# Performance work log

Measured on AMD Instinct MI355X. Metric: run time of the kernel, lower is better.

Reference implementation:

```python
import jax, jax.numpy as jnp
import numpy as np

PADDING = 1
STRIDE = 1


def setup_inputs() -> dict:
    key = jax.random.key(0)
    k1, k2, k3 = jax.random.split(key, 3)
    inputs = jax.random.normal(k1, (32, 128, 56, 56), dtype=jnp.float32)
    weight = jax.random.normal(k2, (256, 128, 3, 3), dtype=jnp.float32) * 0.05
    bias = jax.random.normal(k3, (256,), dtype=jnp.float32) * 0.05
    return {"inputs": inputs, "weight": weight, "bias": bias}


def reference(inputs, weight, bias):
    # Same math as unfold + matmul + fold: a standard 2D convolution
    # (cross-correlation) with bias, NCHW / OIHW layouts.
    out = jax.lax.conv_general_dilated(
        inputs, weight,
        window_strides=(STRIDE, STRIDE),
        padding=[(PADDING, PADDING), (PADDING, PADDING)],
        dimension_numbers=("NCHW", "OIHW", "NCHW"),
    )
    return out + bias[None, :, None, None]
```

## Files before the change

### kernel.cpp

```cpp
#include <hip/hip_runtime.h>
#include <hip/hip_bf16.h>


typedef __bf16 bf16x8 __attribute__((ext_vector_type(8)));
typedef float f32x4 __attribute__((ext_vector_type(4)));

#define N_IMG 32
#define C_IN 128
#define HW 56
#define K_OUT 256
#define YPAD 58
#define XPAD 64
#define IN_PAD_OFF 1048576ul

__device__ __forceinline__ void gl_lds16(const __bf16* g, __bf16* l) {
    __builtin_amdgcn_global_load_lds(
        (const __attribute__((address_space(1))) unsigned int*)(const void*)g,
        (__attribute__((address_space(3))) unsigned int*)(void*)l,
        16, 0, 0);
}

__global__ void prep_weight(const float* __restrict__ wt, __bf16* __restrict__ w2) {
    int idx = blockIdx.x * 256 + threadIdx.x;
    if (idx >= 9 * K_OUT * 16) return;
    int c8 = idx & 15;
    int ko = (idx >> 4) & 255;
    int rs = idx >> 12;
    const float* src = wt + ((size_t)ko * C_IN + c8 * 8) * 9 + rs;
    bf16x8 v8;
#pragma unroll
    for (int k = 0; k < 8; ++k) v8[k] = (__bf16)src[k * 9];
    *(bf16x8*)(w2 + (size_t)idx * 8) = v8;
}

__global__ void prep_input(const float* __restrict__ in, __bf16* __restrict__ in_pad) {
    int bid = blockIdx.x;
    int y = bid % YPAD;
    int n = bid / YPAD;
    int h = y - 1;
    bool interior = (h >= 0 && h < HW);
    __shared__ float tile[HW * 130];
    int t = threadIdx.x;
    if (interior) {
        const float* src = in + (size_t)n * C_IN * (HW * HW) + (size_t)h * HW;
#pragma unroll 1
        for (int idx = t; idx < C_IN * 14; idx += 256) {
            int c = idx / 14, g = idx % 14;
            f32x4 v = *(const f32x4*)(src + (size_t)c * (HW * HW) + g * 4);
            int w = g * 4;
            tile[(w + 0) * 130 + c] = v.x;
            tile[(w + 1) * 130 + c] = v.y;
            tile[(w + 2) * 130 + c] = v.z;
            tile[(w + 3) * 130 + c] = v.w;
        }
    }
    __syncthreads();
    __bf16* dst = in_pad + (size_t)(n * YPAD + y) * XPAD * C_IN;
#pragma unroll 1
    for (int idx = t; idx < XPAD * 16; idx += 256) {
        int x = idx >> 4, cg = idx & 15;
        bf16x8 v8;
        if (interior && x >= 1 && x <= HW) {
            const float* tp = tile + (x - 1) * 130 + cg * 8;
#pragma unroll
            for (int k = 0; k < 8; ++k) v8[k] = (__bf16)tp[k];
        } else {
#pragma unroll
            for (int k = 0; k < 8; ++k) v8[k] = (__bf16)0.f;
        }
        *(bf16x8*)(dst + x * C_IN + cg * 8) = v8;
    }
}

__global__ __launch_bounds__(256, 4) void conv_mfma(
        const __bf16* __restrict__ in_pad,
        const __bf16* __restrict__ w2,
        const float* __restrict__ bias,
        float* __restrict__ out)
{
    __shared__ __bf16 sA[8 * 16 * 64];
    __shared__ __bf16 sB[128 * 64];

    int bid  = blockIdx.x;
    int kot  = bid & 1;
    int wt_  = (bid >> 1) & 3;
    int rest = bid >> 3;
    int ht   = rest % 7;
    int n    = rest / 7;

    int h0  = ht * 8;
    int w0  = (wt_ == 3) ? 40 : wt_ * 16;
    int ko0 = kot * 128;

    int tid  = threadIdx.x;
    int lane = tid & 63;
    int wave = tid >> 6;
    int mw   = wave & 1;
    int nw   = wave >> 1;
    int l15  = lane & 15;
    int quad = lane >> 4;

    int aoff[4], boff[4];
#pragma unroll
    for (int q = 0; q < 4; ++q) {
        int chunk = q * 256 + tid;
        int i  = chunk >> 7;
        int x  = (chunk >> 3) & 15;
        int cs = chunk & 7;
        aoff[q] = (i * XPAD + x) * C_IN + (cs ^ (x & 7)) * 8;
        int ko = chunk >> 3;
        boff[q] = ko * C_IN + (cs ^ (ko & 7)) * 8;
    }

    int ac0   = quad ^ (l15 & 7);
    int aBase = (mw * 64 + l15) * 64;
    int bBase = (nw * 64 + l15) * 64;

    const __bf16* aG = in_pad + (((size_t)n * YPAD + h0) * XPAD + w0) * C_IN;
    const __bf16* bG = w2 + (size_t)ko0 * C_IN;

    f32x4 acc[4][4] = {};

#pragma unroll 1
    for (int r = 0; r < 3; ++r) {
#pragma unroll 1
        for (int s = 0; s < 3; ++s) {
            const __bf16* aStage = aG + (r * XPAD + s) * C_IN;
            const __bf16* bStage = bG + (size_t)(r * 3 + s) * (K_OUT * C_IN);
#pragma unroll 1
            for (int c0 = 0; c0 < C_IN; c0 += 64) {
                __syncthreads();
#pragma unroll
                for (int q = 0; q < 4; ++q)
                    gl_lds16(aStage + c0 + aoff[q], sA + q * 2048 + wave * 512);
#pragma unroll
                for (int q = 0; q < 4; ++q)
                    gl_lds16(bStage + c0 + boff[q], sB + q * 2048 + wave * 512);
                __syncthreads();
#pragma unroll
                for (int ks = 0; ks < 2; ++ks) {
                    int coff = (ac0 ^ (ks << 2)) * 8;
                    bf16x8 a[4], b[4];
#pragma unroll
                    for (int mf = 0; mf < 4; ++mf)
                        a[mf] = *(const bf16x8*)(sA + aBase + mf * 1024 + coff);
#pragma unroll
                    for (int nf = 0; nf < 4; ++nf)
                        b[nf] = *(const bf16x8*)(sB + bBase + nf * 1024 + coff);
#pragma unroll
                    for (int mf = 0; mf < 4; ++mf)
#pragma unroll
                        for (int nf = 0; nf < 4; ++nf)
                            acc[mf][nf] = __builtin_amdgcn_mfma_f32_16x16x32_bf16(
                                a[mf], b[nf], acc[mf][nf], 0, 0, 0);
                }
            }
        }
    }

#pragma unroll
    for (int nf = 0; nf < 4; ++nf) {
        int ko = ko0 + nw * 64 + nf * 16 + l15;
        float bs = bias[ko];
        float* outb = out + (size_t)(n * K_OUT + ko) * (HW * HW)
                          + (size_t)(h0 + mw * 4) * HW + w0 + quad * 4;
#pragma unroll
        for (int mf = 0; mf < 4; ++mf) {
            f32x4 v = acc[mf][nf];
            v = v + bs;
            *(f32x4*)(outb + mf * HW) = v;
        }
    }
}

__global__ void conv_naive(const float* __restrict__ in, const float* __restrict__ wt,
                           const float* __restrict__ bias, float* __restrict__ out) {
    size_t idx = (size_t)blockIdx.x * 256 + threadIdx.x;
    size_t total = (size_t)N_IMG * K_OUT * HW * HW;
    if (idx >= total) return;
    int w  = idx % HW;
    int h  = (idx / HW) % HW;
    int ko = (idx / (HW * HW)) % K_OUT;
    int n  = idx / ((size_t)HW * HW * K_OUT);
    float acc = bias[ko];
    for (int c = 0; c < C_IN; ++c)
        for (int r = 0; r < 3; ++r) {
            int y = h + r - 1;
            if (y < 0 || y >= HW) continue;
            for (int s = 0; s < 3; ++s) {
                int x = w + s - 1;
                if (x < 0 || x >= HW) continue;
                acc += in[((size_t)(n * C_IN + c) * HW + y) * HW + x]
                     * wt[((size_t)ko * C_IN + c) * 9 + r * 3 + s];
            }
        }
    out[idx] = acc;
}

extern "C" void kernel_launch(void* const* d_in, const int* in_sizes, int n_in,
                              void* d_out, int out_size, void* d_ws, size_t ws_size,
                              hipStream_t stream) {
    const float* in   = (const float*)d_in[0];
    const float* wt   = (const float*)d_in[1];
    const float* bias = (const float*)d_in[2];
    float* out = (float*)d_out;

    size_t need = IN_PAD_OFF + (size_t)N_IMG * YPAD * XPAD * C_IN * 2;
    if (ws_size >= need) {
        __bf16* w2     = (__bf16*)d_ws;
        __bf16* in_pad = (__bf16*)((char*)d_ws + IN_PAD_OFF);
        prep_weight<<<(9 * K_OUT * 16 + 255) / 256, 256, 0, stream>>>(wt, w2);
        prep_input<<<N_IMG * YPAD, 256, 0, stream>>>(in, in_pad);
        conv_mfma<<<N_IMG * 7 * 4 * 2, 256, 0, stream>>>(in_pad, w2, bias, out);
    } else {
        size_t total = (size_t)N_IMG * K_OUT * HW * HW;
        conv_naive<<<(unsigned)((total + 255) / 256), 256, 0, stream>>>(in, wt, bias, out);
    }
}
```

Measured before the change: 228.4 us.

## Load halo input tile once into LDS and stream fragment-ordered weights from registers

The conv kernel now loads the whole 10x18 halo tile with all 128 channels into LDS once per block, instead of reloading shifted A tiles for each of the 9 filter taps. The nine taps then read from that single tile by offset, which removes the per-stage syncs. Weights are repacked into MFMA fragment order and read straight from global memory into double-buffered registers, so the B operand no longer goes through LDS. This costs a larger LDS footprint (about 46KB) and more registers, and launch bounds drop from 4 to 3 blocks per CU, so occupancy may fall.

Result: slower. 251.5 us (+10.1%).

```diff
diff --git a/kernel.cpp b/kernel.cpp
--- a/kernel.cpp
+++ b/kernel.cpp
@@ -20,17 +20,24 @@
         16, 0, 0);
 }
 
-__global__ void prep_weight(const float* __restrict__ wt, __bf16* __restrict__ w2) {
+__global__ void prep_weight(const float* __restrict__ wt, __bf16* __restrict__ w3) {
     int idx = blockIdx.x * 256 + threadIdx.x;
-    if (idx >= 9 * K_OUT * 16) return;
-    int c8 = idx & 15;
-    int ko = (idx >> 4) & 255;
-    int rs = idx >> 12;
-    const float* src = wt + ((size_t)ko * C_IN + c8 * 8) * 9 + rs;
-    bf16x8 v8;
-#pragma unroll
-    for (int k = 0; k < 8; ++k) v8[k] = (__bf16)src[k * 9];
-    *(bf16x8*)(w2 + (size_t)idx * 8) = v8;
+    if (idx >= 9 * 2 * 2 * 2 * 2 * 4 * 64) return;
+    int lane = idx & 63;
+    int t = idx >> 6;
+    int nf = t & 3;  t >>= 2;
+    int ks = t & 1;  t >>= 1;
+    int cc = t & 1;  t >>= 1;
+    int nw = t & 1;  t >>= 1;
+    int kot = t & 1; t >>= 1;
+    int rs = t;
+    int ko = kot * 128 + nw * 64 + nf * 16 + (lane & 15);
+    int c0 = cc * 64 + ks * 32 + (lane >> 4) * 8;
+    const float* src = wt + ((size_t)ko * C_IN + c0) * 9 + rs;
+    bf16x8 v;
+#pragma unroll
+    for (int j = 0; j < 8; ++j) v[j] = (__bf16)src[j * 9];
+    *(bf16x8*)(w3 + (size_t)idx * 8) = v;
 }
 
 __global__ void prep_input(const float* __restrict__ in, __bf16* __restrict__ in_pad) {
@@ -72,14 +79,13 @@
     }
 }
 
-__global__ __launch_bounds__(256, 4) void conv_mfma(
+__global__ __launch_bounds__(256, 3) void conv_mfma(
         const __bf16* __restrict__ in_pad,
-        const __bf16* __restrict__ w2,
+        const __bf16* __restrict__ w3,
         const float* __restrict__ bias,
         float* __restrict__ out)
 {
-    __shared__ __bf16 sA[8 * 16 * 64];
-    __shared__ __bf16 sB[128 * 64];
+    __shared__ __align__(16) __bf16 sA[10 * 18 * 128];
 
     int bid  = blockIdx.x;
     int kot  = bid & 1;
@@ -100,61 +106,64 @@
     int l15  = lane & 15;
     int quad = lane >> 4;
 
-    int aoff[4], boff[4];
-#pragma unroll
-    for (int q = 0; q < 4; ++q) {
+    const __bf16* aG = in_pad + (((size_t)n * YPAD + h0) * XPAD + w0) * C_IN;
+
+#pragma unroll
+    for (int q = 0; q < 12; ++q) {
         int chunk = q * 256 + tid;
-        int i  = chunk >> 7;
-        int x  = (chunk >> 3) & 15;
-        int cs = chunk & 7;
-        aoff[q] = (i * XPAD + x) * C_IN + (cs ^ (x & 7)) * 8;
-        int ko = chunk >> 3;
-        boff[q] = ko * C_IN + (cs ^ (ko & 7)) * 8;
-    }
-
-    int ac0   = quad ^ (l15 & 7);
-    int aBase = (mw * 64 + l15) * 64;
-    int bBase = (nw * 64 + l15) * 64;
-
-    const __bf16* aG = in_pad + (((size_t)n * YPAD + h0) * XPAD + w0) * C_IN;
-    const __bf16* bG = w2 + (size_t)ko0 * C_IN;
+        if (chunk < 2880) {
+            int cs = chunk & 15;
+            int xy = chunk >> 4;
+            int x  = xy % 18;
+            int y  = xy / 18;
+            gl_lds16(aG + (y * XPAD + x) * C_IN + ((cs ^ (x & 7)) * 8),
+                     sA + (size_t)(q * 256 + wave * 64) * 8);
+        }
+    }
+
+    const __bf16* bW = w3 + (size_t)(kot * 2 + nw) * 8192 + lane * 8;
+
+    bf16x8 b[2][8];
+#pragma unroll
+    for (int ks = 0; ks < 2; ++ks)
+#pragma unroll
+        for (int nf = 0; nf < 4; ++nf)
+            b[0][ks * 4 + nf] = *(const bf16x8*)(bW + ks * 2048 + nf * 512);
+
+    __syncthreads();
 
     f32x4 acc[4][4] = {};
 
-#pragma unroll 1
-    for (int r = 0; r < 3; ++r) {
-#pragma unroll 1
-        for (int s = 0; s < 3; ++s) {
-            const __bf16* aStage = aG + (r * XPAD + s) * C_IN;
-            const __bf16* bStage = bG + (size_t)(r * 3 + s) * (K_OUT * C_IN);
-#pragma unroll 1
-            for (int c0 = 0; c0 < C_IN; c0 += 64) {
-                __syncthreads();
-#pragma unroll
-                for (int q = 0; q < 4; ++q)
-                    gl_lds16(aStage + c0 + aoff[q], sA + q * 2048 + wave * 512);
-#pragma unroll
-                for (int q = 0; q < 4; ++q)
-                    gl_lds16(bStage + c0 + boff[q], sB + q * 2048 + wave * 512);
-                __syncthreads();
-#pragma unroll
-                for (int ks = 0; ks < 2; ++ks) {
-                    int coff = (ac0 ^ (ks << 2)) * 8;
-                    bf16x8 a[4], b[4];
-#pragma unroll
-                    for (int mf = 0; mf < 4; ++mf)
-                        a[mf] = *(const bf16x8*)(sA + aBase + mf * 1024 + coff);
-#pragma unroll
-                    for (int nf = 0; nf < 4; ++nf)
-                        b[nf] = *(const bf16x8*)(sB + bBase + nf * 1024 + coff);
-#pragma unroll
-                    for (int mf = 0; mf < 4; ++mf)
-#pragma unroll
-                        for (int nf = 0; nf < 4; ++nf)
-                            acc[mf][nf] = __builtin_amdgcn_mfma_f32_16x16x32_bf16(
-                                a[mf], b[nf], acc[mf][nf], 0, 0, 0);
-                }
+#pragma unroll
+    for (int st = 0; st < 18; ++st) {
+        int cc = st / 9, rs = st % 9;
+        if (st < 17) {
+            int ncc = (st + 1) / 9, nrs = (st + 1) % 9;
+#pragma unroll
+            for (int ks = 0; ks < 2; ++ks)
+#pragma unroll
+                for (int nf = 0; nf < 4; ++nf)
+                    b[(st + 1) & 1][ks * 4 + nf] = *(const bf16x8*)
+                        (bW + nrs * 32768 + ncc * 4096 + ks * 2048 + nf * 512);
+        }
+        int r = rs / 3, s = rs % 3;
+        int x = l15 + s;
+        int x7 = x & 7;
+#pragma unroll
+        for (int ks = 0; ks < 2; ++ks) {
+            int slot = (cc * 8 + ks * 4 + quad) ^ x7;
+            bf16x8 a[4];
+#pragma unroll
+            for (int mf = 0; mf < 4; ++mf) {
+                int y = mw * 4 + mf + r;
+                a[mf] = *(const bf16x8*)(sA + (y * 18 + x) * 128 + slot * 8);
             }
+#pragma unroll
+            for (int mf = 0; mf < 4; ++mf)
+#pragma unroll
+                for (int nf = 0; nf < 4; ++nf)
+                    acc[mf][nf] = __builtin_amdgcn_mfma_f32_16x16x32_bf16(
+                        a[mf], b[st & 1][ks * 4 + nf], acc[mf][nf], 0, 0, 0);
         }
     }
 
@@ -207,11 +216,11 @@
 
     size_t need = IN_PAD_OFF + (size_t)N_IMG * YPAD * XPAD * C_IN * 2;
     if (ws_size >= need) {
-        __bf16* w2     = (__bf16*)d_ws;
+        __bf16* w3     = (__bf16*)d_ws;
         __bf16* in_pad = (__bf16*)((char*)d_ws + IN_PAD_OFF);
-        prep_weight<<<(9 * K_OUT * 16 + 255) / 256, 256, 0, stream>>>(wt, w2);
+        prep_weight<<<(9 * 2 * 2 * 2 * 2 * 4 * 64 + 255) / 256, 256, 0, stream>>>(wt, w3);
         prep_input<<<N_IMG * YPAD, 256, 0, stream>>>(in, in_pad);
-        conv_mfma<<<N_IMG * 7 * 4 * 2, 256, 0, stream>>>(in_pad, w2, bias, out);
+        conv_mfma<<<N_IMG * 7 * 4 * 2, 256, 0, stream>>>(in_pad, w3, bias, out);
     } else {
         size_t total = (size_t)N_IMG * K_OUT * HW * HW;
         conv_naive<<<(unsigned)((total + 255) / 256), 256, 0, stream>>>(in, wt, bias, out);
```

## Double-buffer LDS stages in conv MFMA kernel and simplify input transpose indexing

Applied to the files above, without the earlier changes.

The conv kernel's 18 (r,s,c-chunk) stages become one flattened loop with two LDS buffers. The next stage's global-to-LDS loads are issued before computing on the current buffer, so load latency overlaps MFMA work and one barrier per stage is removed. LDS use doubles and launch bounds drop from 4 to 2 blocks per SM, which may reduce occupancy. The input prep loop also replaces the per-iteration div/mod with a fixed channel per thread.

Measured after the change: 252.4 us. 1.11x slower.

```diff
diff --git a/kernel.cpp b/kernel.cpp
--- a/kernel.cpp
+++ b/kernel.cpp
@@ -43,9 +43,10 @@
     int t = threadIdx.x;
     if (interior) {
         const float* src = in + (size_t)n * C_IN * (HW * HW) + (size_t)h * HW;
+        int c  = t & 127;
+        int gg = t >> 7;
 #pragma unroll 1
-        for (int idx = t; idx < C_IN * 14; idx += 256) {
-            int c = idx / 14, g = idx % 14;
+        for (int g = gg; g < 14; g += 2) {
             f32x4 v = *(const f32x4*)(src + (size_t)c * (HW * HW) + g * 4);
             int w = g * 4;
             tile[(w + 0) * 130 + c] = v.x;
@@ -72,14 +73,14 @@
     }
 }
 
-__global__ __launch_bounds__(256, 4) void conv_mfma(
+__global__ __launch_bounds__(256, 2) void conv_mfma(
         const __bf16* __restrict__ in_pad,
         const __bf16* __restrict__ w2,
         const float* __restrict__ bias,
         float* __restrict__ out)
 {
-    __shared__ __bf16 sA[8 * 16 * 64];
-    __shared__ __bf16 sB[128 * 64];
+    __shared__ __align__(16) __bf16 sA[2][8 * 16 * 64];
+    __shared__ __align__(16) __bf16 sB[2][128 * 64];
 
     int bid  = blockIdx.x;
     int kot  = bid & 1;
@@ -121,42 +122,55 @@
 
     f32x4 acc[4][4] = {};
 
+    auto issue = [&](int st, int buf) {
+        int rs = st >> 1;
+        int c0 = (st & 1) << 6;
+        int r = rs / 3, s = rs % 3;
+        const __bf16* aS = aG + (r * XPAD + s) * C_IN + c0;
+        const __bf16* bS = bG + (size_t)rs * (K_OUT * C_IN) + c0;
+#pragma unroll
+        for (int q = 0; q < 4; ++q)
+            gl_lds16(aS + aoff[q], &sA[buf][q * 2048 + wave * 512]);
+#pragma unroll
+        for (int q = 0; q < 4; ++q)
+            gl_lds16(bS + boff[q], &sB[buf][q * 2048 + wave * 512]);
+    };
+
+    auto compute = [&](int buf) {
+#pragma unroll
+        for (int ks = 0; ks < 2; ++ks) {
+            int coff = (ac0 ^ (ks << 2)) * 8;
+            bf16x8 a[4], b[4];
+#pragma unroll
+            for (int mf = 0; mf < 4; ++mf)
+                a[mf] = *(const bf16x8*)(&sA[buf][aBase + mf * 1024 + coff]);
+#pragma unroll
+            for (int nf = 0; nf < 4; ++nf)
+                b[nf] = *(const bf16x8*)(&sB[buf][bBase + nf * 1024 + coff]);
+#pragma unroll
+            for (int mf = 0; mf < 4; ++mf)
+#pragma unroll
+                for (int nf = 0; nf < 4; ++nf)
+                    acc[mf][nf] = __builtin_amdgcn_mfma_f32_16x16x32_bf16(
+                        a[mf], b[nf], acc[mf][nf], 0, 0, 0);
+        }
+    };
+
+    issue(0, 0);
+    __syncthreads();
 #pragma unroll 1
-    for (int r = 0; r < 3; ++r) {
-#pragma unroll 1
-        for (int s = 0; s < 3; ++s) {
-            const __bf16* aStage = aG + (r * XPAD + s) * C_IN;
-            const __bf16* bStage = bG + (size_t)(r * 3 + s) * (K_OUT * C_IN);
-#pragma unroll 1
-            for (int c0 = 0; c0 < C_IN; c0 += 64) {
-                __syncthreads();
-#pragma unroll
-                for (int q = 0; q < 4; ++q)
-                    gl_lds16(aStage + c0 + aoff[q], sA + q * 2048 + wave * 512);
-#pragma unroll
-                for (int q = 0; q < 4; ++q)
-                    gl_lds16(bStage + c0 + boff[q], sB + q * 2048 + wave * 512);
-                __syncthreads();
-#pragma unroll
-                for (int ks = 0; ks < 2; ++ks) {
-                    int coff = (ac0 ^ (ks << 2)) * 8;
-                    bf16x8 a[4], b[4];
-#pragma unroll
-                    for (int mf = 0; mf < 4; ++mf)
-                        a[mf] = *(const bf16x8*)(sA + aBase + mf * 1024 + coff);
-#pragma unroll
-                    for (int nf = 0; nf < 4; ++nf)
-                        b[nf] = *(const bf16x8*)(sB + bBase + nf * 1024 + coff);
-#pragma unroll
-                    for (int mf = 0; mf < 4; ++mf)
-#pragma unroll
-                        for (int nf = 0; nf < 4; ++nf)
-                            acc[mf][nf] = __builtin_amdgcn_mfma_f32_16x16x32_bf16(
-                                a[mf], b[nf], acc[mf][nf], 0, 0, 0);
-                }
-            }
-        }
-    }
+    for (int st = 0; st < 16; st += 2) {
+        issue(st + 1, 1);
+        compute(0);
+        __syncthreads();
+        issue(st + 2, 0);
+        compute(1);
+        __syncthreads();
+    }
+    issue(17, 1);
+    compute(0);
+    __syncthreads();
+    compute(1);
 
 #pragma unroll
     for (int nf = 0; nf < 4; ++nf) {
```
